# Kernel optimization log

Hardware: AMD Instinct MI355X
Metric: run time of the kernel (lower is better)

## Reference

```python
import jax, jax.numpy as jnp
import numpy as np

B, T, S, H, E, V = 32, 32, 64, 512, 512, 32000
NEG = -1e9


def setup_inputs() -> dict:
    key = jax.random.key(0)
    ks = jax.random.split(key, 12)
    g = lambda i, shape: jax.random.normal(ks[i], shape, jnp.float32) * 0.05
    return {
        "tgt_batch": jax.random.randint(ks[0], (B, T), 0, V),
        "len_src_batch": jnp.maximum(jax.random.randint(ks[1], (B,), 0, S), 1),
        "enc_outputs": g(2, (S, B, H)),
        "h0": g(3, (1, B, H)),
        "c0": g(4, (1, B, H)),
        "emb": g(5, (V, E)),
        "W_ih": g(6, (4 * H, E + H)),
        "W_hh": g(7, (4 * H, H)),
        "b_ih": jnp.zeros((4 * H,), jnp.float32),
        "b_hh": jnp.zeros((4 * H,), jnp.float32),
        "W_a": g(8, (H, H)),
        "W_c": g(9, (H, 2 * H)),
        "b_c": jnp.zeros((H,), jnp.float32),
        "W_o": g(10, (V, H)),
        "b_o": jnp.zeros((V,), jnp.float32),
    }


def reference(tgt_batch, len_src_batch, enc_outputs, h0, c0, emb,
              W_ih, W_hh, b_ih, b_hh, W_a, W_c, b_c, W_o, b_o):
    Sv = enc_outputs.shape[0]
    # source padding mask [B,S]
    mask = jnp.arange(Sv)[None, :] < len_src_batch[:, None]
    enc_bsh = enc_outputs.transpose(1, 0, 2)                    # [B,S,H]
    # 'general' attention: score(h,e) = h^T W_a e ; precompute W_a @ e
    proj = jnp.einsum('kh,bsh->bsk', W_a, enc_bsh)              # [B,S,H]
    tgt = tgt_batch.T                                           # [T,B]

    def step(carry, w):
        h, c, ah = carry                                        # each [B,H]
        x = emb[w]                                              # [B,E]
        inp = jnp.concatenate([x, ah], axis=1)                  # [B,E+H]
        gates = inp @ W_ih.T + b_ih + h @ W_hh.T + b_hh         # [B,4H]
        i, f, g, o = jnp.split(gates, 4, axis=1)                # torch gate order
        i, f, o = jax.nn.sigmoid(i), jax.nn.sigmoid(f), jax.nn.sigmoid(o)
        c2 = f * c + i * jnp.tanh(g)
        h2 = o * jnp.tanh(c2)                                   # rnn_output
        scores = jnp.einsum('bk,bsk->bs', h2, proj)
        align = jax.nn.softmax(jnp.where(mask, scores, NEG), axis=1)
        ctx = jnp.einsum('bs,bsh->bh', align, enc_bsh)          # bmm context
        ah2 = jnp.tanh(jnp.concatenate([h2, ctx], axis=1) @ W_c.T + b_c)
        logp = jax.nn.log_softmax(ah2 @ W_o.T + b_o, axis=1)    # [B,V]
        return (h2, c2, ah2), logp

    init = (h0[0], c0[0], jnp.zeros_like(h0[0]))
    _, dec_outputs = jax.lax.scan(step, init, tgt[:-1])         # [T-1,B,V]
    dec_output_words = jnp.argmax(dec_outputs, axis=-1)         # [T-1,B]
    return dec_outputs, dec_output_words
```

## Files before the change

### kernel.cpp

```cpp
#include <hip/hip_runtime.h>
#include <cmath>

#define Bc 32
#define Tc 32
#define Sc 64
#define Hc 512
#define Ec 512
#define Vc 32000
#define NEGC (-1e9f)
#define BH (Bc * Hc)
#define Mtot ((Tc - 1) * Bc)
#define NBLK 256
#define SLOT_PAD 16

__device__ __forceinline__ float sigf(float x) { return 1.0f / (1.0f + expf(-x)); }

__device__ __forceinline__ float dot4(const float* a, const float* b) {
    float4 x = *(const float4*)a;
    float4 y = *(const float4*)b;
    return x.x * y.x + x.y * y.y + x.z * y.z + x.w * y.w;
}

__device__ __forceinline__ void stg(float* p, float v) {
    __hip_atomic_store(p, v, __ATOMIC_RELAXED, __HIP_MEMORY_SCOPE_AGENT);
}

__device__ __forceinline__ void gbar(unsigned int* slots, unsigned int* go,
                                     unsigned int gen) {
    asm volatile("s_waitcnt vmcnt(0)" ::: "memory");
    __syncthreads();
    if (blockIdx.x == 0) {
        int i = threadIdx.x;
        if (i > 0)
            while (__hip_atomic_load(&slots[i * SLOT_PAD], __ATOMIC_RELAXED,
                                     __HIP_MEMORY_SCOPE_AGENT) < gen)
                __builtin_amdgcn_s_sleep(1);
        __syncthreads();
        if (threadIdx.x == 0)
            __hip_atomic_store(go, gen, __ATOMIC_RELAXED, __HIP_MEMORY_SCOPE_AGENT);
    } else {
        if (threadIdx.x == 0) {
            __hip_atomic_store(&slots[blockIdx.x * SLOT_PAD], gen,
                               __ATOMIC_RELAXED, __HIP_MEMORY_SCOPE_AGENT);
            while (__hip_atomic_load(go, __ATOMIC_RELAXED,
                                     __HIP_MEMORY_SCOPE_AGENT) < gen)
                __builtin_amdgcn_s_sleep(1);
        }
        __syncthreads();
    }
    asm volatile("" ::: "memory");
}

__global__ __launch_bounds__(256) void k_proj(const float* __restrict__ W_a,
                                              const float* __restrict__ enc,
                                              float* __restrict__ proj,
                                              unsigned int* __restrict__ bar) {
    if (blockIdx.x == 0 && blockIdx.y == 0 && blockIdx.z == 0) {
        bar[threadIdx.x * SLOT_PAD] = 0u;
        if (threadIdx.x == 0) bar[NBLK * SLOT_PAD] = 0u;
    }
    int k = blockIdx.x * 256 + threadIdx.x;
    int s0 = blockIdx.y * 8;
    int b = blockIdx.z;
    __shared__ float se[8][Hc];
    for (int i = threadIdx.x; i < 8 * Hc; i += 256) {
        int ss = i >> 9, hh = i & (Hc - 1);
        se[ss][hh] = enc[((size_t)(s0 + ss) * Bc + b) * Hc + hh];
    }
    __syncthreads();
    const float* wr = W_a + (size_t)k * Hc;
    float acc[8];
#pragma unroll
    for (int ss = 0; ss < 8; ++ss) acc[ss] = 0.0f;
    for (int h = 0; h < Hc; h += 4) {
        float4 w = *(const float4*)(wr + h);
#pragma unroll
        for (int ss = 0; ss < 8; ++ss) {
            acc[ss] = fmaf(w.x, se[ss][h + 0], acc[ss]);
            acc[ss] = fmaf(w.y, se[ss][h + 1], acc[ss]);
            acc[ss] = fmaf(w.z, se[ss][h + 2], acc[ss]);
            acc[ss] = fmaf(w.w, se[ss][h + 3], acc[ss]);
        }
    }
#pragma unroll
    for (int ss = 0; ss < 8; ++ss)
        proj[((size_t)b * Sc + s0 + ss) * Hc + k] = acc[ss];
}

__global__ __launch_bounds__(256) void k_loop(
    const int* __restrict__ tgt, const int* __restrict__ len_src,
    const float* __restrict__ enc, const float* __restrict__ h0,
    const float* __restrict__ c0, const float* __restrict__ emb,
    const float* __restrict__ W_ih, const float* __restrict__ W_hh,
    const float* __restrict__ b_ih, const float* __restrict__ b_hh,
    const float* __restrict__ proj, const float* __restrict__ W_c,
    const float* __restrict__ b_c,
    float* __restrict__ h_all, float* __restrict__ cbuf,
    float* __restrict__ ah_all, float* __restrict__ ctx_all,
    unsigned int* __restrict__ bar) {
    int blk = blockIdx.x, tid = threadIdx.x;
    unsigned int* slots = bar;
    unsigned int* go = bar + NBLK * SLOT_PAD;
    unsigned int gen = 0;

    {
        int i = blk * 256 + tid;
        if (i < BH) {
            stg(&h_all[i], h0[i]);
            stg(&cbuf[i], c0[i]);
            stg(&ah_all[i], 0.0f);
        }
    }
    gbar(slots, go, ++gen);

    __shared__ float sg[2][4][32];
    __shared__ __align__(16) float sh[Hc];
    __shared__ float ss[Sc];
    __shared__ float sal[Sc];

    for (int t = 0; t < Tc - 1; ++t) {
        const float* hP = h_all + (size_t)t * BH;
        float*       hN = h_all + (size_t)(t + 1) * BH;
        const float* aP = ah_all + (size_t)t * BH;
        float*       aN = ah_all + (size_t)(t + 1) * BH;
        float*       ctxN = ctx_all + (size_t)t * BH;

        {
            int b  = tid & 31;
            int q  = (tid >> 5) & 3;
            int hl = tid >> 7;
            int h  = blk * 2 + hl;
            int j  = q * Hc + h;
            int w  = tgt[b * Tc + t];
            const float* x  = emb + (size_t)w * Ec;
            const float* wi = W_ih + (size_t)j * (Ec + Hc);
            const float* wh = W_hh + (size_t)j * Hc;
            const float* ap = aP + b * Hc;
            const float* hp = hP + b * Hc;
            float a0 = 0.f, a1 = 0.f, a2 = 0.f, a3 = 0.f;
            for (int e = 0; e < Ec; e += 16) {
                a0 += dot4(x + e, wi + e);
                a1 += dot4(x + e + 4, wi + e + 4);
                a2 += dot4(x + e + 8, wi + e + 8);
                a3 += dot4(x + e + 12, wi + e + 12);
            }
            for (int k = 0; k < Hc; k += 16) {
                a0 += dot4(ap + k, wi + Ec + k);
                a1 += dot4(ap + k + 4, wi + Ec + k + 4);
                a2 += dot4(ap + k + 8, wi + Ec + k + 8);
                a3 += dot4(ap + k + 12, wi + Ec + k + 12);
            }
            for (int k = 0; k < Hc; k += 16) {
                a0 += dot4(hp + k, wh + k);
                a1 += dot4(hp + k + 4, wh + k + 4);
                a2 += dot4(hp + k + 8, wh + k + 8);
                a3 += dot4(hp + k + 12, wh + k + 12);
            }
            float acc = b_ih[j] + b_hh[j] + ((a0 + a1) + (a2 + a3));
            sg[hl][q][b] = acc;
            __syncthreads();
            if (q == 0) {
                float iv = sigf(sg[hl][0][b]);
                float fv = sigf(sg[hl][1][b]);
                float gv = tanhf(sg[hl][2][b]);
                float ov = sigf(sg[hl][3][b]);
                int idx = b * Hc + h;
                float c2 = fv * cbuf[idx] + iv * gv;
                float h2v = ov * tanhf(c2);
                cbuf[idx] = c2;
                stg(&hN[idx], h2v);
            }
        }
        gbar(slots, go, ++gen);

        if (blk < Bc) {
            int b = blk;
            for (int k = tid; k < Hc; k += 256) sh[k] = hN[b * Hc + k];
            __syncthreads();
            {
                int s = tid >> 2, r = tid & 3;
                const float* pr = proj + ((size_t)b * Sc + s) * Hc + r * 128;
                const float* hh = sh + r * 128;
                float p0 = 0.f, p1 = 0.f;
                for (int k = 0; k < 128; k += 8) {
                    p0 += dot4(hh + k, pr + k);
                    p1 += dot4(hh + k + 4, pr + k + 4);
                }
                float p = p0 + p1;
                p += __shfl_xor(p, 1);
                p += __shfl_xor(p, 2);
                if (r == 0) ss[s] = p;
            }
            __syncthreads();
            if (tid < Sc) {
                int len = len_src[b];
                float sc = (tid < len) ? ss[tid] : NEGC;
                float mx = sc;
#pragma unroll
                for (int m = 32; m >= 1; m >>= 1) mx = fmaxf(mx, __shfl_xor(mx, m));
                float p = expf(sc - mx);
                float sum = p;
#pragma unroll
                for (int m = 32; m >= 1; m >>= 1) sum += __shfl_xor(sum, m);
                sal[tid] = p / sum;
            }
            __syncthreads();
#pragma unroll
            for (int rep = 0; rep < 2; ++rep) {
                int h = tid + rep * 256;
                float accA = 0.0f, accB = 0.0f;
                for (int s = 0; s < 32; ++s)
                    accA = fmaf(sal[s], enc[((size_t)s * Bc + b) * Hc + h], accA);
                for (int s = 32; s < 64; ++s)
                    accB = fmaf(sal[s], enc[((size_t)s * Bc + b) * Hc + h], accB);
                stg(&ctxN[b * Hc + h], accA + accB);
            }
        }
        gbar(slots, go, ++gen);

        {
            int r   = tid & 3;
            int out = tid >> 2;
            int b   = out >> 1;
            int kl  = out & 1;
            int k   = blk * 2 + kl;
            const float* wc  = W_c + (size_t)k * (2 * Hc) + 4 * r;
            const float* wc2 = wc + Hc;
            const float* hp  = hN + b * Hc + 4 * r;
            const float* cp  = ctxN + b * Hc + 4 * r;
            float ar = 0.f;
            for (int j = 0; j < Hc; j += 16)
                ar += dot4(hp + j, wc + j);
            for (int j = 0; j < Hc; j += 16)
                ar += dot4(cp + j, wc2 + j);
            float v01 = ar + __shfl_xor(ar, 1);
            float v   = v01 + __shfl_xor(v01, 2);
            if (r == 0)
                stg(&aN[b * Hc + k], tanhf(b_c[k] + v));
        }
        gbar(slots, go, ++gen);
    }
}

__global__ __launch_bounds__(256) void k_biglogits(const float* __restrict__ A,
                                                   const float* __restrict__ W_o,
                                                   const float* __restrict__ b_o,
                                                   float* __restrict__ out) {
    __shared__ float At[32][128];
    __shared__ float Bt[32][128];
    int tid = threadIdx.x;
    int n_base = blockIdx.x * 128;
    int m_base = blockIdx.y * 128;
    int tn = tid & 15, tm = tid >> 4;

    float acc[2][4][2][4];
#pragma unroll
    for (int mg = 0; mg < 2; ++mg)
#pragma unroll
        for (int mi = 0; mi < 4; ++mi)
#pragma unroll
            for (int ng = 0; ng < 2; ++ng)
#pragma unroll
                for (int ni = 0; ni < 4; ++ni) acc[mg][mi][ng][ni] = 0.0f;

    int srow = tid >> 1;
    int koff = (tid & 1) * 16;
    int gm = m_base + srow;
    const float* arow = A + (size_t)gm * Hc + koff;
    const float* brow = W_o + (size_t)(n_base + srow) * Hc + koff;

    for (int kc = 0; kc < Hc; kc += 32) {
        float av[16], bv[16];
#pragma unroll
        for (int i = 0; i < 4; ++i) {
            float4 t4 = (gm < Mtot) ? *(const float4*)(arow + kc + i * 4)
                                    : make_float4(0.f, 0.f, 0.f, 0.f);
            av[i * 4 + 0] = t4.x; av[i * 4 + 1] = t4.y; av[i * 4 + 2] = t4.z; av[i * 4 + 3] = t4.w;
            float4 u4 = *(const float4*)(brow + kc + i * 4);
            bv[i * 4 + 0] = u4.x; bv[i * 4 + 1] = u4.y; bv[i * 4 + 2] = u4.z; bv[i * 4 + 3] = u4.w;
        }
        __syncthreads();
#pragma unroll
        for (int i = 0; i < 16; ++i) {
            At[koff + i][srow] = av[i];
            Bt[koff + i][srow] = bv[i];
        }
        __syncthreads();
#pragma unroll
        for (int k = 0; k < 32; ++k) {
            float4 a0 = *(const float4*)&At[k][tm * 4];
            float4 a1 = *(const float4*)&At[k][64 + tm * 4];
            float4 b0 = *(const float4*)&Bt[k][tn * 4];
            float4 b1 = *(const float4*)&Bt[k][64 + tn * 4];
            float am[2][4] = {{a0.x, a0.y, a0.z, a0.w}, {a1.x, a1.y, a1.z, a1.w}};
            float bn[2][4] = {{b0.x, b0.y, b0.z, b0.w}, {b1.x, b1.y, b1.z, b1.w}};
#pragma unroll
            for (int mg = 0; mg < 2; ++mg)
#pragma unroll
                for (int mi = 0; mi < 4; ++mi)
#pragma unroll
                    for (int ng = 0; ng < 2; ++ng)
#pragma unroll
                        for (int ni = 0; ni < 4; ++ni)
                            acc[mg][mi][ng][ni] = fmaf(am[mg][mi], bn[ng][ni], acc[mg][mi][ng][ni]);
        }
        __syncthreads();
    }

#pragma unroll
    for (int ng = 0; ng < 2; ++ng) {
        int n = n_base + ng * 64 + tn * 4;
        float4 bo = *(const float4*)(b_o + n);
#pragma unroll
        for (int mg = 0; mg < 2; ++mg)
#pragma unroll
            for (int mi = 0; mi < 4; ++mi) {
                int m = m_base + mg * 64 + tm * 4 + mi;
                if (m < Mtot) {
                    float4 v;
                    v.x = acc[mg][mi][ng][0] + bo.x;
                    v.y = acc[mg][mi][ng][1] + bo.y;
                    v.z = acc[mg][mi][ng][2] + bo.z;
                    v.w = acc[mg][mi][ng][3] + bo.w;
                    *(float4*)(out + (size_t)m * Vc + n) = v;
                }
            }
    }
}

__global__ __launch_bounds__(256) void k_reduce_norm(float* __restrict__ out,
                                                     float* __restrict__ words) {
    int m = blockIdx.x, tid = threadIdx.x;
    float* row = out + (size_t)m * Vc;
    float mx = -INFINITY;
    int mi = 0;
    for (int v = tid; v < Vc; v += 256) {
        float x = row[v];
        if (x > mx) { mx = x; mi = v; }
    }
    __shared__ float smx[256];
    __shared__ int smi[256];
    __shared__ float ssum[256];
    smx[tid] = mx; smi[tid] = mi;
    __syncthreads();
    for (int off = 128; off; off >>= 1) {
        if (tid < off) {
            float o = smx[tid + off]; int oi = smi[tid + off];
            if (o > smx[tid] || (o == smx[tid] && oi < smi[tid])) { smx[tid] = o; smi[tid] = oi; }
        }
        __syncthreads();
    }
    float gmx = smx[0];
    float s = 0.0f;
    for (int v = tid; v < Vc; v += 256) s += expf(row[v] - gmx);
    ssum[tid] = s;
    __syncthreads();
    for (int off = 128; off; off >>= 1) {
        if (tid < off) ssum[tid] += ssum[tid + off];
        __syncthreads();
    }
    float lse = gmx + logf(ssum[0]);
    __syncthreads();
    for (int v = tid; v < Vc; v += 256) row[v] -= lse;
    if (tid == 0) words[m] = (float)smi[0];
}

extern "C" void kernel_launch(void* const* d_in, const int* in_sizes, int n_in,
                              void* d_out, int out_size, void* d_ws, size_t ws_size,
                              hipStream_t stream) {
    const int*   tgt     = (const int*)d_in[0];
    const int*   len_src = (const int*)d_in[1];
    const float* enc     = (const float*)d_in[2];
    const float* h0      = (const float*)d_in[3];
    const float* c0      = (const float*)d_in[4];
    const float* emb     = (const float*)d_in[5];
    const float* W_ih    = (const float*)d_in[6];
    const float* W_hh    = (const float*)d_in[7];
    const float* b_ih    = (const float*)d_in[8];
    const float* b_hh    = (const float*)d_in[9];
    const float* W_a     = (const float*)d_in[10];
    const float* W_c     = (const float*)d_in[11];
    const float* b_c     = (const float*)d_in[12];
    const float* W_o     = (const float*)d_in[13];
    const float* b_o     = (const float*)d_in[14];

    float* out = (float*)d_out;
    float* ws = (float*)d_ws;

    float* proj    = ws;
    float* h_all   = proj + (size_t)Bc * Sc * Hc;
    float* cbuf    = h_all + 32 * (size_t)BH;
    float* ah_all  = cbuf + BH;
    float* ctx_all = ah_all + 32 * (size_t)BH;
    unsigned int* bar = (unsigned int*)(ctx_all + 31 * (size_t)BH);
    float* out_words = out + (size_t)(Tc - 1) * Bc * Vc;

    {
        dim3 g(Hc / 256, Sc / 8, Bc);
        k_proj<<<g, 256, 0, stream>>>(W_a, enc, proj, bar);
    }

    k_loop<<<NBLK, 256, 0, stream>>>(tgt, len_src, enc, h0, c0, emb,
                                     W_ih, W_hh, b_ih, b_hh, proj, W_c, b_c,
                                     h_all, cbuf, ah_all, ctx_all, bar);

    {
        dim3 g(Vc / 128, (Mtot + 127) / 128);
        k_biglogits<<<g, 256, 0, stream>>>(ah_all + BH, W_o, b_o, out);
    }
    k_reduce_norm<<<Mtot, 256, 0, stream>>>(out, out_words);
}
```

Baseline: 3.428 ms.

## Replace centralized grid barrier with all-to-all flag polling and batch dot-product loads

The grid barrier is changed from a master-block gather/release scheme to one where every block publishes its generation flag and each thread of every block polls one peer's flag. This removes the serial two-hop latency of the coordinator. The cost is 256x256 concurrent polls on padded slots. Separately, the LSTM gate and W_c dot-product loops now issue eight or four float4 loads before the FMAs, to increase memory-level parallelism in the latency-bound recurrent step.

New measurement: 3.749 ms. +9.4%, slower.

```diff
diff --git a/kernel.cpp b/kernel.cpp
--- a/kernel.cpp
+++ b/kernel.cpp
@@ -11,7 +11,7 @@
 #define BH (Bc * Hc)
 #define Mtot ((Tc - 1) * Bc)
 #define NBLK 256
-#define SLOT_PAD 16
+#define SLOT_PAD 32
 
 __device__ __forceinline__ float sigf(float x) { return 1.0f / (1.0f + expf(-x)); }
 
@@ -21,33 +21,24 @@
     return x.x * y.x + x.y * y.y + x.z * y.z + x.w * y.w;
 }
 
+__device__ __forceinline__ float d4v(float4 x, float4 y) {
+    return x.x * y.x + x.y * y.y + x.z * y.z + x.w * y.w;
+}
+
 __device__ __forceinline__ void stg(float* p, float v) {
     __hip_atomic_store(p, v, __ATOMIC_RELAXED, __HIP_MEMORY_SCOPE_AGENT);
 }
 
-__device__ __forceinline__ void gbar(unsigned int* slots, unsigned int* go,
-                                     unsigned int gen) {
+__device__ __forceinline__ void gbar(unsigned int* slots, unsigned int gen) {
     asm volatile("s_waitcnt vmcnt(0)" ::: "memory");
     __syncthreads();
-    if (blockIdx.x == 0) {
-        int i = threadIdx.x;
-        if (i > 0)
-            while (__hip_atomic_load(&slots[i * SLOT_PAD], __ATOMIC_RELAXED,
-                                     __HIP_MEMORY_SCOPE_AGENT) < gen)
-                __builtin_amdgcn_s_sleep(1);
-        __syncthreads();
-        if (threadIdx.x == 0)
-            __hip_atomic_store(go, gen, __ATOMIC_RELAXED, __HIP_MEMORY_SCOPE_AGENT);
-    } else {
-        if (threadIdx.x == 0) {
-            __hip_atomic_store(&slots[blockIdx.x * SLOT_PAD], gen,
-                               __ATOMIC_RELAXED, __HIP_MEMORY_SCOPE_AGENT);
-            while (__hip_atomic_load(go, __ATOMIC_RELAXED,
-                                     __HIP_MEMORY_SCOPE_AGENT) < gen)
-                __builtin_amdgcn_s_sleep(1);
-        }
-        __syncthreads();
-    }
+    if (threadIdx.x == 0)
+        __hip_atomic_store(&slots[blockIdx.x * SLOT_PAD], gen,
+                           __ATOMIC_RELAXED, __HIP_MEMORY_SCOPE_AGENT);
+    const unsigned int* p = &slots[threadIdx.x * SLOT_PAD];
+    while (__hip_atomic_load(p, __ATOMIC_RELAXED, __HIP_MEMORY_SCOPE_AGENT) < gen)
+        __builtin_amdgcn_s_sleep(1);
+    __syncthreads();
     asm volatile("" ::: "memory");
 }
 
@@ -55,10 +46,8 @@
                                               const float* __restrict__ enc,
                                               float* __restrict__ proj,
                                               unsigned int* __restrict__ bar) {
-    if (blockIdx.x == 0 && blockIdx.y == 0 && blockIdx.z == 0) {
+    if (blockIdx.x == 0 && blockIdx.y == 0 && blockIdx.z == 0)
         bar[threadIdx.x * SLOT_PAD] = 0u;
-        if (threadIdx.x == 0) bar[NBLK * SLOT_PAD] = 0u;
-    }
     int k = blockIdx.x * 256 + threadIdx.x;
     int s0 = blockIdx.y * 8;
     int b = blockIdx.z;
@@ -99,8 +88,6 @@
     float* __restrict__ ah_all, float* __restrict__ ctx_all,
     unsigned int* __restrict__ bar) {
     int blk = blockIdx.x, tid = threadIdx.x;
-    unsigned int* slots = bar;
-    unsigned int* go = bar + NBLK * SLOT_PAD;
     unsigned int gen = 0;
 
     {
@@ -111,7 +98,7 @@
             stg(&ah_all[i], 0.0f);
         }
     }
-    gbar(slots, go, ++gen);
+    gbar(bar, ++gen);
 
     __shared__ float sg[2][4][32];
     __shared__ __align__(16) float sh[Hc];
@@ -138,23 +125,41 @@
             const float* ap = aP + b * Hc;
             const float* hp = hP + b * Hc;
             float a0 = 0.f, a1 = 0.f, a2 = 0.f, a3 = 0.f;
-            for (int e = 0; e < Ec; e += 16) {
-                a0 += dot4(x + e, wi + e);
-                a1 += dot4(x + e + 4, wi + e + 4);
-                a2 += dot4(x + e + 8, wi + e + 8);
-                a3 += dot4(x + e + 12, wi + e + 12);
-            }
-            for (int k = 0; k < Hc; k += 16) {
-                a0 += dot4(ap + k, wi + Ec + k);
-                a1 += dot4(ap + k + 4, wi + Ec + k + 4);
-                a2 += dot4(ap + k + 8, wi + Ec + k + 8);
-                a3 += dot4(ap + k + 12, wi + Ec + k + 12);
-            }
-            for (int k = 0; k < Hc; k += 16) {
-                a0 += dot4(hp + k, wh + k);
-                a1 += dot4(hp + k + 4, wh + k + 4);
-                a2 += dot4(hp + k + 8, wh + k + 8);
-                a3 += dot4(hp + k + 12, wh + k + 12);
+            for (int e = 0; e < Ec; e += 32) {
+                float4 xv[8], wv[8];
+#pragma unroll
+                for (int i = 0; i < 8; ++i) {
+                    xv[i] = *(const float4*)(x + e + 4 * i);
+                    wv[i] = *(const float4*)(wi + e + 4 * i);
+                }
+                a0 += d4v(xv[0], wv[0]); a1 += d4v(xv[1], wv[1]);
+                a2 += d4v(xv[2], wv[2]); a3 += d4v(xv[3], wv[3]);
+                a0 += d4v(xv[4], wv[4]); a1 += d4v(xv[5], wv[5]);
+                a2 += d4v(xv[6], wv[6]); a3 += d4v(xv[7], wv[7]);
+            }
+            for (int k = 0; k < Hc; k += 32) {
+                float4 xv[8], wv[8];
+#pragma unroll
+                for (int i = 0; i < 8; ++i) {
+                    xv[i] = *(const float4*)(ap + k + 4 * i);
+                    wv[i] = *(const float4*)(wi + Ec + k + 4 * i);
+                }
+                a0 += d4v(xv[0], wv[0]); a1 += d4v(xv[1], wv[1]);
+                a2 += d4v(xv[2], wv[2]); a3 += d4v(xv[3], wv[3]);
+                a0 += d4v(xv[4], wv[4]); a1 += d4v(xv[5], wv[5]);
+                a2 += d4v(xv[6], wv[6]); a3 += d4v(xv[7], wv[7]);
+            }
+            for (int k = 0; k < Hc; k += 32) {
+                float4 xv[8], wv[8];
+#pragma unroll
+                for (int i = 0; i < 8; ++i) {
+                    xv[i] = *(const float4*)(hp + k + 4 * i);
+                    wv[i] = *(const float4*)(wh + k + 4 * i);
+                }
+                a0 += d4v(xv[0], wv[0]); a1 += d4v(xv[1], wv[1]);
+                a2 += d4v(xv[2], wv[2]); a3 += d4v(xv[3], wv[3]);
+                a0 += d4v(xv[4], wv[4]); a1 += d4v(xv[5], wv[5]);
+                a2 += d4v(xv[6], wv[6]); a3 += d4v(xv[7], wv[7]);
             }
             float acc = b_ih[j] + b_hh[j] + ((a0 + a1) + (a2 + a3));
             sg[hl][q][b] = acc;
@@ -171,7 +176,7 @@
                 stg(&hN[idx], h2v);
             }
         }
-        gbar(slots, go, ++gen);
+        gbar(bar, ++gen);
 
         if (blk < Bc) {
             int b = blk;
@@ -216,7 +221,7 @@
                 stg(&ctxN[b * Hc + h], accA + accB);
             }
         }
-        gbar(slots, go, ++gen);
+        gbar(bar, ++gen);
 
         {
             int r   = tid & 3;
@@ -229,16 +234,32 @@
             const float* hp  = hN + b * Hc + 4 * r;
             const float* cp  = ctxN + b * Hc + 4 * r;
             float ar = 0.f;
-            for (int j = 0; j < Hc; j += 16)
-                ar += dot4(hp + j, wc + j);
-            for (int j = 0; j < Hc; j += 16)
-                ar += dot4(cp + j, wc2 + j);
+            for (int j = 0; j < Hc; j += 64) {
+                float4 hv[4], wv[4];
+#pragma unroll
+                for (int i = 0; i < 4; ++i) {
+                    hv[i] = *(const float4*)(hp + j + 16 * i);
+                    wv[i] = *(const float4*)(wc + j + 16 * i);
+                }
+                ar += d4v(hv[0], wv[0]); ar += d4v(hv[1], wv[1]);
+                ar += d4v(hv[2], wv[2]); ar += d4v(hv[3], wv[3]);
+            }
+            for (int j = 0; j < Hc; j += 64) {
+                float4 hv[4], wv[4];
+#pragma unroll
+                for (int i = 0; i < 4; ++i) {
+                    hv[i] = *(const float4*)(cp + j + 16 * i);
+                    wv[i] = *(const float4*)(wc2 + j + 16 * i);
+                }
+                ar += d4v(hv[0], wv[0]); ar += d4v(hv[1], wv[1]);
+                ar += d4v(hv[2], wv[2]); ar += d4v(hv[3], wv[3]);
+            }
             float v01 = ar + __shfl_xor(ar, 1);
             float v   = v01 + __shfl_xor(v01, 2);
             if (r == 0)
                 stg(&aN[b * Hc + k], tanhf(b_c[k] + v));
         }
-        gbar(slots, go, ++gen);
+        gbar(bar, ++gen);
     }
 }
 
```
